# Kernel tuning notes

Measured on AMD Instinct MI355X. Metric: run time of the kernel, lower is better.

The kernel has to match this reference:

```python
import jax, jax.numpy as jnp
import numpy as np

NUM_HEADS = 16
THETA = 1000.0


def apply_rope(x, positions, theta):
    """x: [B, H, S, d_k]; positions: [S] float. Interleaved-pair RoPE."""
    d = x.shape[-1]
    inv_freq = theta ** (-jnp.arange(0, d, 2, dtype=x.dtype) / d)  # [d/2]
    ang = positions[:, None] * inv_freq[None, :]                    # [S, d/2]
    cos, sin = jnp.cos(ang), jnp.sin(ang)
    x1, x2 = x[..., 0::2], x[..., 1::2]
    r1 = x1 * cos - x2 * sin
    r2 = x1 * sin + x2 * cos
    return jnp.stack([r1, r2], axis=-1).reshape(x.shape)


def setup_inputs() -> dict:
    key = jax.random.key(0)
    ks = jax.random.split(key, 5)
    B, S, D = 2, 2048, 1024
    scale = 1.0 / np.sqrt(D)
    return {
        "in_features": jax.random.normal(ks[0], (B, S, D), jnp.float32),
        "q_proj_weight": jax.random.normal(ks[1], (D, D), jnp.float32) * scale,
        "k_proj_weight": jax.random.normal(ks[2], (D, D), jnp.float32) * scale,
        "v_proj_weight": jax.random.normal(ks[3], (D, D), jnp.float32) * scale,
        "o_proj_weight": jax.random.normal(ks[4], (D, D), jnp.float32) * scale,
        "token_positions": jnp.arange(S, dtype=jnp.int32),
    }


def reference(in_features, q_proj_weight, k_proj_weight, v_proj_weight,
              o_proj_weight, token_positions):
    B, S, D = in_features.shape
    H = NUM_HEADS
    d_k = D // H

    # Original rearrange: '(d_k heads) d_model -> heads d_model d_k'
    # => first dim splits as [d_k, heads] (heads is the inner factor).
    def split_heads(w):
        return w.reshape(d_k, H, D).transpose(1, 2, 0)  # [H, D, d_k]

    Wq, Wk, Wv = split_heads(q_proj_weight), split_heads(k_proj_weight), split_heads(v_proj_weight)

    xq = jnp.einsum("bsd,hdk->bhsk", in_features, Wq)
    xk = jnp.einsum("bsd,hdk->bhsk", in_features, Wk)
    xv = jnp.einsum("bsd,hdk->bhsk", in_features, Wv)

    pos = token_positions.astype(in_features.dtype)
    xq = apply_rope(xq, pos, THETA)
    xk = apply_rope(xk, pos, THETA)

    scores = jnp.einsum("bhqk,bhmk->bhqm", xq, xk) / jnp.sqrt(
        jnp.asarray(d_k, in_features.dtype))
    causal_mask = jnp.triu(jnp.ones((S, S), bool), k=1)  # True above diagonal
    scores = jnp.where(causal_mask, -jnp.inf, scores)
    attn = jax.nn.softmax(scores, axis=-1)

    out = jnp.einsum("bhqm,bhmv->bhqv", attn, xv)        # [B, H, S, d_k]
    out = out.transpose(0, 2, 1, 3).reshape(B, S, D)     # (heads d_emb) concat
    return out @ o_proj_weight                            # [B, S, d_o]
```

## Files before the change

### kernel.cpp

```cpp
#include <hip/hip_runtime.h>

typedef unsigned short u16;
typedef unsigned int u32;
typedef __bf16 bf16x8 __attribute__((ext_vector_type(8)));
typedef float f32x4 __attribute__((ext_vector_type(4)));

#define SEQ 2048
#define DMODEL 1024
#define NH 16
#define DK 64
#define BATCH 2
#define MTOT (BATCH * SEQ)

__device__ __forceinline__ u16 f2b(float f) {
  u32 u = __float_as_uint(f);
  u += 0x7fffu + ((u >> 16) & 1u);
  return (u16)(u >> 16);
}

__device__ __forceinline__ void gload16(const void* g, void* l) {
  __builtin_amdgcn_global_load_lds((const __attribute__((address_space(1))) u32*)g,
                                   (__attribute__((address_space(3))) u32*)l, 16, 0, 0);
}

__global__ __launch_bounds__(256) void cvt_bf16(const float* __restrict__ in,
                                                u16* __restrict__ out, int n4) {
  int i = blockIdx.x * 256 + threadIdx.x;
  if (i < n4) {
    float4 v = ((const float4*)in)[i];
    uint2 o;
    o.x = (u32)f2b(v.x) | ((u32)f2b(v.y) << 16);
    o.y = (u32)f2b(v.z) | ((u32)f2b(v.w) << 16);
    ((uint2*)out)[i] = o;
  }
}

__global__ __launch_bounds__(256) void cvt_w3(const float* __restrict__ wq,
                                              const float* __restrict__ wk,
                                              const float* __restrict__ wv,
                                              u16* __restrict__ oq,
                                              u16* __restrict__ ok,
                                              u16* __restrict__ ov) {
  const int m = blockIdx.y;
  const float* in = (m == 0) ? wq : ((m == 1) ? wk : wv);
  u16* out = (m == 0) ? oq : ((m == 1) ? ok : ov);
  const int i = blockIdx.x * 256 + threadIdx.x;
  float4 v = ((const float4*)in)[i];
  uint2 o;
  o.x = (u32)f2b(v.x) | ((u32)f2b(v.y) << 16);
  o.y = (u32)f2b(v.z) | ((u32)f2b(v.w) << 16);
  ((uint2*)out)[i] = o;
}

__global__ __launch_bounds__(256) void rope_tab_k(const int* __restrict__ tokpos,
                                                  float2* __restrict__ tab) {
  const int i = blockIdx.x * 256 + threadIdx.x;
  const int s = i >> 5, Xi = i & 31;
  const float invf = powf(1000.0f, -(float)Xi / 32.0f);
  const float ang = (float)tokpos[s] * invf;
  float sn, cs;
  sincosf(ang, &sn, &cs);
  tab[i] = make_float2(cs, sn);
}

__global__ __launch_bounds__(256) void transpose_wo(const float* __restrict__ wo,
                                                    u16* __restrict__ wot) {
  __shared__ float tile[32][33];
  const int bx = blockIdx.x * 32;
  const int by = blockIdx.y * 32;
  const int tx = threadIdx.x & 31, ty = threadIdx.x >> 5;
  for (int j = ty; j < 32; j += 8)
    tile[j][tx] = wo[(size_t)(by + j) * DMODEL + bx + tx];
  __syncthreads();
  for (int j = ty; j < 32; j += 8)
    wot[(size_t)(bx + j) * DMODEL + by + tx] = f2b(tile[tx][j]);
}

__device__ __forceinline__ void qkv_core(const u16* __restrict__ A,
                                         const u16* __restrict__ Bt,
                                         int mbase, int nbase,
                                         u16* As, u16* Bs, f32x4 acc[4][4]) {
  const int t = threadIdx.x;
  const int lane = t & 63, w = t >> 6;
  const int wr = w >> 1, wc = w & 1;
  const int l15 = lane & 15, lg = lane >> 4;
  const int srow = t >> 3;
  const int sch = (t & 7) ^ (srow & 7);
  const int rsw = l15 & 7;
  const int ASZ = 128 * 64;
  const int NIT = DMODEL / 64;

  auto stage = [&](int bufsel, int kb) {
    u16* Ad = &As[bufsel * ASZ];
    u16* Bd = &Bs[bufsel * ASZ];
#pragma unroll
    for (int j = 0; j < 4; ++j)
      gload16(&A[(size_t)(mbase + srow + 32 * j) * DMODEL + kb + sch * 8],
              &Ad[j * 2048 + t * 8]);
#pragma unroll
    for (int j = 0; j < 4; ++j)
      gload16(&Bt[(size_t)(nbase + srow + 32 * j) * DMODEL + kb + sch * 8],
              &Bd[j * 2048 + t * 8]);
  };

  auto compute = [&](int bufsel) {
    const u16* Ac = &As[bufsel * ASZ];
    const u16* Bc = &Bs[bufsel * ASZ];
#pragma unroll
    for (int kk = 0; kk < 2; ++kk) {
      bf16x8 af[4], bfr[4];
#pragma unroll
      for (int mi = 0; mi < 4; ++mi) {
        const int row = wr * 64 + mi * 16 + l15;
        af[mi] = *(const bf16x8*)&Ac[row * 64 + (((kk * 4 + lg) ^ rsw) * 8)];
      }
#pragma unroll
      for (int ni = 0; ni < 4; ++ni) {
        const int row = wc * 64 + ni * 16 + l15;
        bfr[ni] = *(const bf16x8*)&Bc[row * 64 + (((kk * 4 + lg) ^ rsw) * 8)];
      }
#pragma unroll
      for (int mi = 0; mi < 4; ++mi)
#pragma unroll
        for (int ni = 0; ni < 4; ++ni)
          acc[mi][ni] =
              __builtin_amdgcn_mfma_f32_16x16x32_bf16(af[mi], bfr[ni], acc[mi][ni], 0, 0, 0);
    }
  };

  stage(0, 0);

  for (int it = 0; it < NIT - 1; ++it) {
    const int buf = it & 1;
    stage(buf ^ 1, (it + 1) * 64);
    __builtin_amdgcn_sched_barrier(0);
    asm volatile("s_waitcnt vmcnt(8)" ::: "memory");
    __builtin_amdgcn_sched_barrier(0);
    __builtin_amdgcn_s_barrier();
    __builtin_amdgcn_sched_barrier(0);
    compute(buf);
    __builtin_amdgcn_sched_barrier(0);
    __builtin_amdgcn_s_barrier();
  }
  asm volatile("s_waitcnt vmcnt(0)" ::: "memory");
  __builtin_amdgcn_sched_barrier(0);
  __builtin_amdgcn_s_barrier();
  __builtin_amdgcn_sched_barrier(0);
  compute((DMODEL / 64 - 1) & 1);
}

__global__ __launch_bounds__(256) void gemm_qkv(
    const u16* __restrict__ Xb, const u16* __restrict__ Wqb,
    const u16* __restrict__ Wkb, const u16* __restrict__ Wvb,
    u16* __restrict__ Qb, u16* __restrict__ Kb, u16* __restrict__ Vb,
    const float2* __restrict__ tab) {
  __shared__ __align__(16) u16 As[2 * 128 * 64];
  __shared__ __align__(16) u16 Bs[2 * 128 * 64];

  const int mat = blockIdx.y >> 3;
  const int nbase = (blockIdx.y & 7) * 128;
  const int mbase = blockIdx.x * 128;
  const u16* Bt = (mat == 0) ? Wqb : ((mat == 1) ? Wkb : Wvb);

  f32x4 acc[4][4];
#pragma unroll
  for (int mi = 0; mi < 4; ++mi)
#pragma unroll
    for (int ni = 0; ni < 4; ++ni) {
      f32x4 z = {0.f, 0.f, 0.f, 0.f};
      acc[mi][ni] = z;
    }

  qkv_core(Xb, Bt, mbase, nbase, As, Bs, acc);

  const int t = threadIdx.x;
  const int lane = t & 63, w = t >> 6;
  const int wr = w >> 1, wc = w & 1;
  const int l15 = lane & 15, lg = lane >> 4;

  if (mat == 2) {
#pragma unroll
    for (int mi = 0; mi < 4; ++mi) {
#pragma unroll
      for (int r = 0; r < 4; ++r) {
        const int row = mbase + wr * 64 + mi * 16 + lg * 4 + r;
        const int bi = row >> 11, s = row & (SEQ - 1);
#pragma unroll
        for (int ni = 0; ni < 4; ++ni) {
          const int c = nbase + wc * 64 + ni * 16 + l15;
          const int hh = c & 15, vd = c >> 4;
          Vb[((size_t)((bi * NH + hh) * DK + vd)) * SEQ + s] = f2b(acc[mi][ni][r]);
        }
      }
    }
  } else {
    u16* Ob = (mat == 0) ? Qb : Kb;
    const float qscale = (mat == 0) ? 0.125f * 1.44269504088896f : 1.0f;
#pragma unroll
    for (int ni = 0; ni < 4; ni += 2) {
      const int Xi = (nbase + wc * 64 + ni * 16) >> 5;
#pragma unroll
      for (int mi = 0; mi < 4; ++mi) {
#pragma unroll
        for (int r = 0; r < 4; ++r) {
          const int row = mbase + wr * 64 + mi * 16 + lg * 4 + r;
          const int bi = row >> 11, s = row & (SEQ - 1);
          const float2 ct = tab[(s << 5) + Xi];
          const float x1 = acc[mi][ni][r], x2 = acc[mi][ni + 1][r];
          const float r1 = (x1 * ct.x - x2 * ct.y) * qscale;
          const float r2 = (x1 * ct.y + x2 * ct.x) * qscale;
          const u32 pk = (u32)f2b(r1) | ((u32)f2b(r2) << 16);
          *(u32*)&Ob[((size_t)((bi * NH + l15) * SEQ + s) << 6) + (Xi << 1)] = pk;
        }
      }
    }
  }
}

__global__ __launch_bounds__(256) void flash_attn(
    const u16* __restrict__ Qg, const u16* __restrict__ Kg,
    const u16* __restrict__ VTg, u16* __restrict__ Ag) {
  __shared__ __align__(16) u16 Ks[2][64 * 64];
  __shared__ __align__(16) u16 Vs[2][64 * 64];
  __shared__ __align__(16) u16 Ps[4][16][72];

  const int id = blockIdx.y * 32 + blockIdx.x;
  const int within = id >> 3;
  const int bh = (id & 7) * 4 + (within & 3);
  const int qt = 31 - (within >> 2);
  const int b = bh >> 4, h = bh & 15;
  const int qbase = qt * 64;

  const size_t hoff = (size_t)bh * SEQ * DK;
  const u16* Qh = Qg + hoff;
  const u16* Kh = Kg + hoff;
  const u16* VTh = VTg + hoff;

  const int t = threadIdx.x;
  const int lane = t & 63, w = t >> 6;
  const int l15 = lane & 15, lg = lane >> 4;
  const int sw = l15 & 7;

  const int qrow = qbase + w * 16 + l15;
  const bf16x8 qf0 = *(const bf16x8*)&Qh[(size_t)qrow * DK + lg * 8];
  const bf16x8 qf1 = *(const bf16x8*)&Qh[(size_t)qrow * DK + 32 + lg * 8];

  f32x4 oaccT[4];
#pragma unroll
  for (int vf = 0; vf < 4; ++vf) {
    f32x4 z = {0.f, 0.f, 0.f, 0.f};
    oaccT[vf] = z;
  }
  float m_r = -1e30f, l_r = 0.0f;

  const int srow = t >> 3;
  const int sc = ((t & 7) ^ (srow & 7)) * 8;

  auto stageKV = [&](int bufsel, int kb) {
    gload16(&Kh[(size_t)(kb + srow) * DK + sc], &Ks[bufsel][t * 8]);
    gload16(&Kh[(size_t)(kb + srow + 32) * DK + sc], &Ks[bufsel][2048 + t * 8]);
    gload16(&VTh[(size_t)srow * SEQ + kb + sc], &Vs[bufsel][t * 8]);
    gload16(&VTh[(size_t)(srow + 32) * SEQ + kb + sc], &Vs[bufsel][2048 + t * 8]);
  };

  stageKV(0, 0);

  for (int kt = 0; kt <= qt; ++kt) {
    const int buf = kt & 1;
    if (kt < qt) {
      stageKV(buf ^ 1, (kt + 1) * 64);
      __builtin_amdgcn_sched_barrier(0);
      asm volatile("s_waitcnt vmcnt(4)" ::: "memory");
    } else {
      __builtin_amdgcn_sched_barrier(0);
      asm volatile("s_waitcnt vmcnt(0)" ::: "memory");
    }
    __builtin_amdgcn_sched_barrier(0);
    __builtin_amdgcn_s_barrier();
    __builtin_amdgcn_sched_barrier(0);

    const int kvbase = kt * 64;

    f32x4 sT[4];
    __builtin_amdgcn_s_setprio(1);
#pragma unroll
    for (int f = 0; f < 4; ++f) {
      const int row = f * 16 + l15;
      bf16x8 k0 = *(const bf16x8*)&Ks[buf][row * 64 + (lg ^ sw) * 8];
      bf16x8 k1 = *(const bf16x8*)&Ks[buf][row * 64 + ((4 + lg) ^ sw) * 8];
      f32x4 z = {0.f, 0.f, 0.f, 0.f};
      z = __builtin_amdgcn_mfma_f32_16x16x32_bf16(k0, qf0, z, 0, 0, 0);
      z = __builtin_amdgcn_mfma_f32_16x16x32_bf16(k1, qf1, z, 0, 0, 0);
      sT[f] = z;
    }
    __builtin_amdgcn_s_setprio(0);

    if (kt == qt) {
#pragma unroll
      for (int f = 0; f < 4; ++f)
#pragma unroll
        for (int r = 0; r < 4; ++r) {
          const int kvc = kvbase + f * 16 + lg * 4 + r;
          if (kvc > qrow) sT[f][r] = -1e30f;
        }
    }

    f32x4 mv;
#pragma unroll
    for (int r = 0; r < 4; ++r)
      mv[r] = fmaxf(fmaxf(sT[0][r], sT[1][r]), fmaxf(sT[2][r], sT[3][r]));
    float mx = fmaxf(fmaxf(mv[0], mv[1]), fmaxf(mv[2], mv[3]));
    mx = fmaxf(mx, __shfl_xor(mx, 16));
    mx = fmaxf(mx, __shfl_xor(mx, 32));

    const float mn = fmaxf(m_r, mx);
    const float alpha = exp2f(m_r - mn);
    m_r = mn;
#pragma unroll
    for (int f = 0; f < 4; ++f)
#pragma unroll
      for (int r = 0; r < 4; ++r) sT[f][r] = exp2f(sT[f][r] - mn);

    f32x4 rv;
#pragma unroll
    for (int r = 0; r < 4; ++r) rv[r] = (sT[0][r] + sT[1][r]) + (sT[2][r] + sT[3][r]);
    float rs = (rv[0] + rv[1]) + (rv[2] + rv[3]);
    rs += __shfl_xor(rs, 16);
    rs += __shfl_xor(rs, 32);
    l_r = l_r * alpha + rs;

#pragma unroll
    for (int vf = 0; vf < 4; ++vf)
#pragma unroll
      for (int r = 0; r < 4; ++r) oaccT[vf][r] *= alpha;

#pragma unroll
    for (int f = 0; f < 4; ++f) {
      uint2 pkv;
      pkv.x = (u32)f2b(sT[f][0]) | ((u32)f2b(sT[f][1]) << 16);
      pkv.y = (u32)f2b(sT[f][2]) | ((u32)f2b(sT[f][3]) << 16);
      *(uint2*)&Ps[w][l15][f * 16 + lg * 4] = pkv;
    }

    __builtin_amdgcn_s_setprio(1);
#pragma unroll
    for (int c = 0; c < 2; ++c) {
      const bf16x8 pb = *(const bf16x8*)&Ps[w][l15][c * 32 + lg * 8];
#pragma unroll
      for (int vf = 0; vf < 4; ++vf) {
        const bf16x8 va =
            *(const bf16x8*)&Vs[buf][(vf * 16 + l15) * 64 + ((c * 4 + lg) ^ sw) * 8];
        oaccT[vf] = __builtin_amdgcn_mfma_f32_16x16x32_bf16(va, pb, oaccT[vf], 0, 0, 0);
      }
    }
    __builtin_amdgcn_s_setprio(0);

    __builtin_amdgcn_sched_barrier(0);
    __builtin_amdgcn_s_barrier();
  }

  const float inv = 1.0f / l_r;
  const size_t base = ((size_t)(b * SEQ + qrow)) * DMODEL + h * DK;
#pragma unroll
  for (int vf = 0; vf < 4; ++vf) {
    uint2 ov;
    ov.x = (u32)f2b(oaccT[vf][0] * inv) | ((u32)f2b(oaccT[vf][1] * inv) << 16);
    ov.y = (u32)f2b(oaccT[vf][2] * inv) | ((u32)f2b(oaccT[vf][3] * inv) << 16);
    *(uint2*)&Ag[base + vf * 16 + lg * 4] = ov;
  }
}

__global__ __launch_bounds__(256) void gemm_out(const u16* __restrict__ Ab,
                                                const u16* __restrict__ Wotb,
                                                float* __restrict__ Co) {
  __shared__ __align__(16) u16 As[64 * 64];
  __shared__ __align__(16) u16 Bs[128 * 64];
  const int mbase = blockIdx.x * 64, nbase = blockIdx.y * 128;

  const int t = threadIdx.x;
  const int lane = t & 63, w = t >> 6;
  const int wr = w >> 1, wc = w & 1;
  const int l15 = lane & 15, lg = lane >> 4;
  const int srow = t >> 3;
  const int sch = (t & 7) ^ (srow & 7);
  const int rsw = l15 & 7;

  f32x4 acc[2][4];
#pragma unroll
  for (int mi = 0; mi < 2; ++mi)
#pragma unroll
    for (int ni = 0; ni < 4; ++ni) {
      f32x4 z = {0.f, 0.f, 0.f, 0.f};
      acc[mi][ni] = z;
    }

  for (int kb = 0; kb < DMODEL; kb += 64) {
    gload16(&Ab[(size_t)(mbase + srow) * DMODEL + kb + sch * 8], &As[t * 8]);
    gload16(&Ab[(size_t)(mbase + 32 + srow) * DMODEL + kb + sch * 8], &As[2048 + t * 8]);
#pragma unroll
    for (int j = 0; j < 4; ++j)
      gload16(&Wotb[(size_t)(nbase + srow + 32 * j) * DMODEL + kb + sch * 8],
              &Bs[j * 2048 + t * 8]);
    __syncthreads();
#pragma unroll
    for (int kk = 0; kk < 2; ++kk) {
      bf16x8 af[2], bfr[4];
#pragma unroll
      for (int mi = 0; mi < 2; ++mi) {
        const int row = wr * 32 + mi * 16 + l15;
        af[mi] = *(const bf16x8*)&As[row * 64 + (((kk * 4 + lg) ^ rsw) * 8)];
      }
#pragma unroll
      for (int ni = 0; ni < 4; ++ni) {
        const int row = wc * 64 + ni * 16 + l15;
        bfr[ni] = *(const bf16x8*)&Bs[row * 64 + (((kk * 4 + lg) ^ rsw) * 8)];
      }
#pragma unroll
      for (int mi = 0; mi < 2; ++mi)
#pragma unroll
        for (int ni = 0; ni < 4; ++ni)
          acc[mi][ni] =
              __builtin_amdgcn_mfma_f32_16x16x32_bf16(af[mi], bfr[ni], acc[mi][ni], 0, 0, 0);
    }
    __syncthreads();
  }

#pragma unroll
  for (int mi = 0; mi < 2; ++mi) {
#pragma unroll
    for (int r = 0; r < 4; ++r) {
      const int row = mbase + wr * 32 + mi * 16 + lg * 4 + r;
#pragma unroll
      for (int ni = 0; ni < 4; ++ni) {
        const int c = nbase + wc * 64 + ni * 16 + l15;
        Co[(size_t)row * DMODEL + c] = acc[mi][ni][r];
      }
    }
  }
}

extern "C" void kernel_launch(void* const* d_in, const int* in_sizes, int n_in,
                              void* d_out, int out_size, void* d_ws, size_t ws_size,
                              hipStream_t stream) {
  const float* X = (const float*)d_in[0];
  const float* Wq = (const float*)d_in[1];
  const float* Wk = (const float*)d_in[2];
  const float* Wv = (const float*)d_in[3];
  const float* Wo = (const float*)d_in[4];
  const int* tokpos = (const int*)d_in[5];
  float* out = (float*)d_out;

  u16* p = (u16*)d_ws;
  u16* Xb = p;   p += (size_t)MTOT * DMODEL;
  u16* Wqb = p;  p += (size_t)DMODEL * DMODEL;
  u16* Wkb = p;  p += (size_t)DMODEL * DMODEL;
  u16* Wvb = p;  p += (size_t)DMODEL * DMODEL;
  u16* Wotb = p; p += (size_t)DMODEL * DMODEL;
  u16* Qb = p;   p += (size_t)BATCH * NH * SEQ * DK;
  u16* Kb = p;   p += (size_t)BATCH * NH * SEQ * DK;
  u16* Vb = p;   p += (size_t)BATCH * NH * SEQ * DK;
  float2* tab = (float2*)(p + 512);
  u16* Ab = Xb;

  cvt_bf16<<<4096, 256, 0, stream>>>(X, Xb, (MTOT * DMODEL) / 4);
  cvt_w3<<<dim3(1024, 3), 256, 0, stream>>>(Wq, Wk, Wv, Wqb, Wkb, Wvb);
  transpose_wo<<<dim3(32, 32), 256, 0, stream>>>(Wo, Wotb);
  rope_tab_k<<<(SEQ * 32) / 256, 256, 0, stream>>>(tokpos, tab);

  gemm_qkv<<<dim3(32, 24), 256, 0, stream>>>(Xb, Wqb, Wkb, Wvb, Qb, Kb, Vb, tab);
  flash_attn<<<dim3(32, 32), 256, 0, stream>>>(Qb, Kb, Vb, Ab);
  gemm_out<<<dim3(64, 8), 256, 0, stream>>>(Ab, Wotb, out);
}
```

Before: 142.4 us.

## Process 128 query rows per flash-attention block, two 16-row groups per wave

The flash attention kernel now handles a 128-row query tile per block, with each wave owning two 16-row groups. K fragments loaded from LDS are reused across both groups, and each staged K/V tile serves twice as many queries, halving global K/V traffic per query. Causal masking skips fully masked groups per tile. The grid is halved to 512 blocks, which lowers parallelism and raises register pressure from the doubled accumulators and softmax state.

```diff
diff --git a/kernel.cpp b/kernel.cpp
--- a/kernel.cpp
+++ b/kernel.cpp
@@ -222,14 +222,14 @@
     const u16* __restrict__ VTg, u16* __restrict__ Ag) {
   __shared__ __align__(16) u16 Ks[2][64 * 64];
   __shared__ __align__(16) u16 Vs[2][64 * 64];
-  __shared__ __align__(16) u16 Ps[4][16][72];
-
-  const int id = blockIdx.y * 32 + blockIdx.x;
+  __shared__ __align__(16) u16 Ps[4][2][16][72];
+
+  const int id = blockIdx.y * 16 + blockIdx.x;
   const int within = id >> 3;
   const int bh = (id & 7) * 4 + (within & 3);
-  const int qt = 31 - (within >> 2);
+  const int qt = 15 - (within >> 2);
   const int b = bh >> 4, h = bh & 15;
-  const int qbase = qt * 64;
+  const int qbase = qt * 128;
 
   const size_t hoff = (size_t)bh * SEQ * DK;
   const u16* Qh = Qg + hoff;
@@ -241,17 +241,28 @@
   const int l15 = lane & 15, lg = lane >> 4;
   const int sw = l15 & 7;
 
-  const int qrow = qbase + w * 16 + l15;
-  const bf16x8 qf0 = *(const bf16x8*)&Qh[(size_t)qrow * DK + lg * 8];
-  const bf16x8 qf1 = *(const bf16x8*)&Qh[(size_t)qrow * DK + 32 + lg * 8];
-
-  f32x4 oaccT[4];
-#pragma unroll
-  for (int vf = 0; vf < 4; ++vf) {
-    f32x4 z = {0.f, 0.f, 0.f, 0.f};
-    oaccT[vf] = z;
-  }
-  float m_r = -1e30f, l_r = 0.0f;
+  const int gb0 = qbase + w * 32;
+
+  bf16x8 qf[2][2];
+#pragma unroll
+  for (int g = 0; g < 2; ++g) {
+    const int qrow = gb0 + g * 16 + l15;
+    qf[g][0] = *(const bf16x8*)&Qh[(size_t)qrow * DK + lg * 8];
+    qf[g][1] = *(const bf16x8*)&Qh[(size_t)qrow * DK + 32 + lg * 8];
+  }
+
+  f32x4 oaccT[2][4];
+  float m_r[2], l_r[2];
+#pragma unroll
+  for (int g = 0; g < 2; ++g) {
+    m_r[g] = -1e30f;
+    l_r[g] = 0.0f;
+#pragma unroll
+    for (int vf = 0; vf < 4; ++vf) {
+      f32x4 z = {0.f, 0.f, 0.f, 0.f};
+      oaccT[g][vf] = z;
+    }
+  }
 
   const int srow = t >> 3;
   const int sc = ((t & 7) ^ (srow & 7)) * 8;
@@ -265,9 +276,11 @@
 
   stageKV(0, 0);
 
-  for (int kt = 0; kt <= qt; ++kt) {
+  const int ktmax = 2 * qt + 1;
+
+  for (int kt = 0; kt <= ktmax; ++kt) {
     const int buf = kt & 1;
-    if (kt < qt) {
+    if (kt < ktmax) {
       stageKV(buf ^ 1, (kt + 1) * 64);
       __builtin_amdgcn_sched_barrier(0);
       asm volatile("s_waitcnt vmcnt(4)" ::: "memory");
@@ -280,93 +293,118 @@
     __builtin_amdgcn_sched_barrier(0);
 
     const int kvbase = kt * 64;
-
-    f32x4 sT[4];
-    __builtin_amdgcn_s_setprio(1);
-#pragma unroll
-    for (int f = 0; f < 4; ++f) {
-      const int row = f * 16 + l15;
-      bf16x8 k0 = *(const bf16x8*)&Ks[buf][row * 64 + (lg ^ sw) * 8];
-      bf16x8 k1 = *(const bf16x8*)&Ks[buf][row * 64 + ((4 + lg) ^ sw) * 8];
-      f32x4 z = {0.f, 0.f, 0.f, 0.f};
-      z = __builtin_amdgcn_mfma_f32_16x16x32_bf16(k0, qf0, z, 0, 0, 0);
-      z = __builtin_amdgcn_mfma_f32_16x16x32_bf16(k1, qf1, z, 0, 0, 0);
-      sT[f] = z;
-    }
-    __builtin_amdgcn_s_setprio(0);
-
-    if (kt == qt) {
-#pragma unroll
-      for (int f = 0; f < 4; ++f)
-#pragma unroll
-        for (int r = 0; r < 4; ++r) {
-          const int kvc = kvbase + f * 16 + lg * 4 + r;
-          if (kvc > qrow) sT[f][r] = -1e30f;
+    const bool act0 = kvbase <= gb0 + 15;
+    const bool act1 = kvbase <= gb0 + 31;
+
+    if (act1) {
+      bf16x8 kf0[4], kf1[4];
+#pragma unroll
+      for (int f = 0; f < 4; ++f) {
+        const int row = f * 16 + l15;
+        kf0[f] = *(const bf16x8*)&Ks[buf][row * 64 + (lg ^ sw) * 8];
+        kf1[f] = *(const bf16x8*)&Ks[buf][row * 64 + ((4 + lg) ^ sw) * 8];
+      }
+
+#pragma unroll
+      for (int g = 0; g < 2; ++g) {
+        const int gbase = gb0 + g * 16;
+        const bool act = (g == 0) ? act0 : act1;
+        if (!act) continue;
+        const int qrow = gbase + l15;
+
+        f32x4 sT[4];
+        __builtin_amdgcn_s_setprio(1);
+#pragma unroll
+        for (int f = 0; f < 4; ++f) {
+          f32x4 z = {0.f, 0.f, 0.f, 0.f};
+          z = __builtin_amdgcn_mfma_f32_16x16x32_bf16(kf0[f], qf[g][0], z, 0, 0, 0);
+          z = __builtin_amdgcn_mfma_f32_16x16x32_bf16(kf1[f], qf[g][1], z, 0, 0, 0);
+          sT[f] = z;
         }
-    }
-
-    f32x4 mv;
-#pragma unroll
-    for (int r = 0; r < 4; ++r)
-      mv[r] = fmaxf(fmaxf(sT[0][r], sT[1][r]), fmaxf(sT[2][r], sT[3][r]));
-    float mx = fmaxf(fmaxf(mv[0], mv[1]), fmaxf(mv[2], mv[3]));
-    mx = fmaxf(mx, __shfl_xor(mx, 16));
-    mx = fmaxf(mx, __shfl_xor(mx, 32));
-
-    const float mn = fmaxf(m_r, mx);
-    const float alpha = exp2f(m_r - mn);
-    m_r = mn;
-#pragma unroll
-    for (int f = 0; f < 4; ++f)
-#pragma unroll
-      for (int r = 0; r < 4; ++r) sT[f][r] = exp2f(sT[f][r] - mn);
-
-    f32x4 rv;
-#pragma unroll
-    for (int r = 0; r < 4; ++r) rv[r] = (sT[0][r] + sT[1][r]) + (sT[2][r] + sT[3][r]);
-    float rs = (rv[0] + rv[1]) + (rv[2] + rv[3]);
-    rs += __shfl_xor(rs, 16);
-    rs += __shfl_xor(rs, 32);
-    l_r = l_r * alpha + rs;
-
-#pragma unroll
-    for (int vf = 0; vf < 4; ++vf)
-#pragma unroll
-      for (int r = 0; r < 4; ++r) oaccT[vf][r] *= alpha;
-
-#pragma unroll
-    for (int f = 0; f < 4; ++f) {
-      uint2 pkv;
-      pkv.x = (u32)f2b(sT[f][0]) | ((u32)f2b(sT[f][1]) << 16);
-      pkv.y = (u32)f2b(sT[f][2]) | ((u32)f2b(sT[f][3]) << 16);
-      *(uint2*)&Ps[w][l15][f * 16 + lg * 4] = pkv;
-    }
-
-    __builtin_amdgcn_s_setprio(1);
-#pragma unroll
-    for (int c = 0; c < 2; ++c) {
-      const bf16x8 pb = *(const bf16x8*)&Ps[w][l15][c * 32 + lg * 8];
-#pragma unroll
-      for (int vf = 0; vf < 4; ++vf) {
-        const bf16x8 va =
-            *(const bf16x8*)&Vs[buf][(vf * 16 + l15) * 64 + ((c * 4 + lg) ^ sw) * 8];
-        oaccT[vf] = __builtin_amdgcn_mfma_f32_16x16x32_bf16(va, pb, oaccT[vf], 0, 0, 0);
-      }
-    }
-    __builtin_amdgcn_s_setprio(0);
+        __builtin_amdgcn_s_setprio(0);
+
+        if (kvbase + 63 > gbase) {
+#pragma unroll
+          for (int f = 0; f < 4; ++f)
+#pragma unroll
+            for (int r = 0; r < 4; ++r) {
+              const int kvc = kvbase + f * 16 + lg * 4 + r;
+              if (kvc > qrow) sT[f][r] = -1e30f;
+            }
+        }
+
+        f32x4 mv;
+#pragma unroll
+        for (int r = 0; r < 4; ++r)
+          mv[r] = fmaxf(fmaxf(sT[0][r], sT[1][r]), fmaxf(sT[2][r], sT[3][r]));
+        float mx = fmaxf(fmaxf(mv[0], mv[1]), fmaxf(mv[2], mv[3]));
+        mx = fmaxf(mx, __shfl_xor(mx, 16));
+        mx = fmaxf(mx, __shfl_xor(mx, 32));
+
+        const float mn = fmaxf(m_r[g], mx);
+        const float alpha = exp2f(m_r[g] - mn);
+        m_r[g] = mn;
+#pragma unroll
+        for (int f = 0; f < 4; ++f)
+#pragma unroll
+          for (int r = 0; r < 4; ++r) sT[f][r] = exp2f(sT[f][r] - mn);
+
+        f32x4 rv;
+#pragma unroll
+        for (int r = 0; r < 4; ++r)
+          rv[r] = (sT[0][r] + sT[1][r]) + (sT[2][r] + sT[3][r]);
+        float rs = (rv[0] + rv[1]) + (rv[2] + rv[3]);
+        rs += __shfl_xor(rs, 16);
+        rs += __shfl_xor(rs, 32);
+        l_r[g] = l_r[g] * alpha + rs;
+
+#pragma unroll
+        for (int vf = 0; vf < 4; ++vf)
+#pragma unroll
+          for (int r = 0; r < 4; ++r) oaccT[g][vf][r] *= alpha;
+
+#pragma unroll
+        for (int f = 0; f < 4; ++f) {
+          uint2 pkv;
+          pkv.x = (u32)f2b(sT[f][0]) | ((u32)f2b(sT[f][1]) << 16);
+          pkv.y = (u32)f2b(sT[f][2]) | ((u32)f2b(sT[f][3]) << 16);
+          *(uint2*)&Ps[w][g][l15][f * 16 + lg * 4] = pkv;
+        }
+      }
+
+      __builtin_amdgcn_s_setprio(1);
+#pragma unroll
+      for (int c = 0; c < 2; ++c) {
+        const bf16x8 pb0 = *(const bf16x8*)&Ps[w][0][l15][c * 32 + lg * 8];
+        const bf16x8 pb1 = *(const bf16x8*)&Ps[w][1][l15][c * 32 + lg * 8];
+#pragma unroll
+        for (int vf = 0; vf < 4; ++vf) {
+          const bf16x8 va =
+              *(const bf16x8*)&Vs[buf][(vf * 16 + l15) * 64 + ((c * 4 + lg) ^ sw) * 8];
+          if (act0)
+            oaccT[0][vf] = __builtin_amdgcn_mfma_f32_16x16x32_bf16(va, pb0, oaccT[0][vf], 0, 0, 0);
+          oaccT[1][vf] = __builtin_amdgcn_mfma_f32_16x16x32_bf16(va, pb1, oaccT[1][vf], 0, 0, 0);
+        }
+      }
+      __builtin_amdgcn_s_setprio(0);
+    }
 
     __builtin_amdgcn_sched_barrier(0);
     __builtin_amdgcn_s_barrier();
   }
 
-  const float inv = 1.0f / l_r;
-  const size_t base = ((size_t)(b * SEQ + qrow)) * DMODEL + h * DK;
-#pragma unroll
-  for (int vf = 0; vf < 4; ++vf) {
-    uint2 ov;
-    ov.x = (u32)f2b(oaccT[vf][0] * inv) | ((u32)f2b(oaccT[vf][1] * inv) << 16);
-    ov.y = (u32)f2b(oaccT[vf][2] * inv) | ((u32)f2b(oaccT[vf][3] * inv) << 16);
-    *(uint2*)&Ag[base + vf * 16 + lg * 4] = ov;
+#pragma unroll
+  for (int g = 0; g < 2; ++g) {
+    const float inv = 1.0f / l_r[g];
+    const int qrow = gb0 + g * 16 + l15;
+    const size_t base = ((size_t)(b * SEQ + qrow)) * DMODEL + h * DK;
+#pragma unroll
+    for (int vf = 0; vf < 4; ++vf) {
+      uint2 ov;
+      ov.x = (u32)f2b(oaccT[g][vf][0] * inv) | ((u32)f2b(oaccT[g][vf][1] * inv) << 16);
+      ov.y = (u32)f2b(oaccT[g][vf][2] * inv) | ((u32)f2b(oaccT[g][vf][3] * inv) << 16);
+      *(uint2*)&Ag[base + vf * 16 + lg * 4] = ov;
+    }
   }
 }
 
@@ -468,6 +506,6 @@
   rope_tab_k<<<(SEQ * 32) / 256, 256, 0, stream>>>(tokpos, tab);
 
   gemm_qkv<<<dim3(32, 24), 256, 0, stream>>>(Xb, Wqb, Wkb, Wvb, Qb, Kb, Vb, tab);
-  flash_attn<<<dim3(32, 32), 256, 0, stream>>>(Qb, Kb, Vb, Ab);
+  flash_attn<<<dim3(16, 32), 256, 0, stream>>>(Qb, Kb, Vb, Ab);
   gemm_out<<<dim3(64, 8), 256, 0, stream>>>(Ab, Wotb, out);
 }
```

Result: slower. 170.5 us (+19.8%).
